# Performance work log

Hardware: AMD Instinct MI355X
Metric: run time of the kernel (lower is better)

The kernel has to match this reference:

```python
import jax, jax.numpy as jnp
import numpy as np

DIM = 1024
HEADS = 16
DIM_HEAD = 64
SCALE = DIM_HEAD ** -0.5
LN_EPS = 1e-5


def rotate_half(x):
    # '... (j d) -> ... j d' with j=2, then cat(-x2, x1)
    d = x.shape[-1] // 2
    x1, x2 = x[..., :d], x[..., d:]
    return jnp.concatenate((-x2, x1), axis=-1)


def apply_rotary_pos_emb(pos, t):
    seq_len, rotate_dim = t.shape[-2], pos.shape[-1]
    pos = pos[..., -seq_len:, :]
    t_rot, t_pass = t[..., :rotate_dim], t[..., rotate_dim:]
    t_rot = t_rot * jnp.cos(pos) + rotate_half(t_rot) * jnp.sin(pos)
    return jnp.concatenate((t_rot, t_pass), axis=-1)


def setup_inputs() -> dict:
    key = jax.random.key(0)
    ks = jax.random.split(key, 4)
    b, n = 2, 2048
    inner = HEADS * DIM_HEAD
    x = jax.random.normal(ks[0], (b, n, DIM), dtype=jnp.float32)
    rotary_pos_emb = jax.random.normal(ks[1], (n, DIM_HEAD), dtype=jnp.float32)
    # params (torch Linear stored transposed here as [in, out])
    w_qkv = jax.random.normal(ks[2], (DIM, inner * 3), dtype=jnp.float32) * (DIM ** -0.5)
    w_out = jax.random.normal(ks[3], (inner, DIM), dtype=jnp.float32) * (inner ** -0.5)
    ln_w = jnp.ones((DIM,), dtype=jnp.float32)
    ln_b = jnp.zeros((DIM,), dtype=jnp.float32)
    return {"x": x, "rotary_pos_emb": rotary_pos_emb, "ln_w": ln_w, "ln_b": ln_b,
            "w_qkv": w_qkv, "w_out": w_out}


def reference(x, rotary_pos_emb, ln_w, ln_b, w_qkv, w_out):
    b, n, _ = x.shape
    # LayerNorm
    mu = jnp.mean(x, axis=-1, keepdims=True)
    var = jnp.mean(jnp.square(x - mu), axis=-1, keepdims=True)
    xn = (x - mu) * jax.lax.rsqrt(var + LN_EPS) * ln_w + ln_b
    # QKV projection
    qkv = xn @ w_qkv  # [b, n, 3*inner]
    q, k, v = jnp.split(qkv, 3, axis=-1)
    split_heads = lambda t: t.reshape(b, n, HEADS, DIM_HEAD).transpose(0, 2, 1, 3)
    q, k, v = split_heads(q), split_heads(k), split_heads(v)  # [b, h, n, d]
    q = q * SCALE
    q = apply_rotary_pos_emb(rotary_pos_emb, q)
    k = apply_rotary_pos_emb(rotary_pos_emb, k)
    sim = jnp.einsum('bhid,bhjd->bhij', q, k)
    causal_mask = jnp.triu(jnp.ones((n, n), dtype=bool), k=1)
    sim = jnp.where(causal_mask, -jnp.finfo(sim.dtype).max, sim)
    attn = jax.nn.softmax(sim, axis=-1)
    out = jnp.einsum('bhij,bhjd->bhid', attn, v)
    out = out.transpose(0, 2, 1, 3).reshape(b, n, HEADS * DIM_HEAD)
    return out @ w_out
```

## Files before the change

kernel.cpp:

```cpp
#include <hip/hip_runtime.h>
#include <hip/hip_bf16.h>

typedef __bf16 bf16;
typedef __attribute__((ext_vector_type(8))) __bf16 bf16x8;
typedef __attribute__((ext_vector_type(4))) __bf16 bf16x4;
typedef __attribute__((ext_vector_type(4))) float f32x4;
typedef __attribute__((ext_vector_type(16))) float f32x16;
typedef __attribute__((ext_vector_type(2))) int int2v;
typedef __attribute__((ext_vector_type(4))) int int4v;

#define HEADS 16
#define DHEAD 64
#define SEQ 2048
#define DIMM 1024
#define QKVN (3*DIMM)
#define SCALEQ 0.125f

__device__ __forceinline__ void gload_lds16(const bf16* g, bf16* l) {
  __builtin_amdgcn_global_load_lds(
      (const __attribute__((address_space(1))) void*)g,
      (__attribute__((address_space(3))) void*)l, 16, 0, 0);
}

__device__ __forceinline__ f32x16 mfma32(bf16x8 a, bf16x8 b, f32x16 c) {
  return __builtin_amdgcn_mfma_f32_32x32x16_bf16(a, b, c, 0, 0, 0);
}

__device__ __forceinline__ unsigned cvtpk(float a, float b) {
  unsigned r;
  asm("v_cvt_pk_bf16_f32 %0, %1, %2" : "=v"(r) : "v"(a), "v"(b));
  return r;
}

__global__ __launch_bounds__(256) void transpose_cast_k(const float* __restrict__ in,
                                                        bf16* __restrict__ out, int R, int C) {
  __shared__ bf16 tile[32][33];
  int bc = blockIdx.x, br = blockIdx.y;
  int t = threadIdx.x;
  int c = t & 31, r0 = t >> 5;
  for (int i = 0; i < 4; i++) {
    int r = r0 + i * 8;
    tile[r][c] = (bf16)in[(size_t)(br * 32 + r) * C + bc * 32 + c];
  }
  __syncthreads();
  for (int i = 0; i < 4; i++) {
    int r = r0 + i * 8;
    out[(size_t)(bc * 32 + r) * R + br * 32 + c] = tile[c][r];
  }
}

__global__ void rope_table_k(const float* __restrict__ pos, float2* __restrict__ cs) {
  int i = blockIdx.x * 256 + threadIdx.x;
  float p = pos[i];
  cs[i] = make_float2(cosf(p), sinf(p));
}

__global__ __launch_bounds__(256) void ln_k(const float* __restrict__ x, const float* __restrict__ w,
                                            const float* __restrict__ bsh, bf16* __restrict__ xn) {
  int row = blockIdx.x, t = threadIdx.x;
  const float4 v = reinterpret_cast<const float4*>(x + (size_t)row * DIMM)[t];
  float s1 = v.x + v.y + v.z + v.w;
  float s2 = v.x * v.x + v.y * v.y + v.z * v.z + v.w * v.w;
  for (int off = 1; off < 64; off <<= 1) {
    s1 += __shfl_xor(s1, off, 64);
    s2 += __shfl_xor(s2, off, 64);
  }
  __shared__ float red[8];
  int wv = t >> 6;
  if ((t & 63) == 0) { red[wv * 2] = s1; red[wv * 2 + 1] = s2; }
  __syncthreads();
  s1 = red[0] + red[2] + red[4] + red[6];
  s2 = red[1] + red[3] + red[5] + red[7];
  float mu = s1 * (1.0f / DIMM);
  float var = s2 * (1.0f / DIMM) - mu * mu;
  float rs = rsqrtf(var + 1e-5f);
  const float4 wv4 = reinterpret_cast<const float4*>(w)[t];
  const float4 bv4 = reinterpret_cast<const float4*>(bsh)[t];
  bf16x4 o;
  o[0] = (bf16)((v.x - mu) * rs * wv4.x + bv4.x);
  o[1] = (bf16)((v.y - mu) * rs * wv4.y + bv4.y);
  o[2] = (bf16)((v.z - mu) * rs * wv4.z + bv4.z);
  o[3] = (bf16)((v.w - mu) * rs * wv4.w + bv4.w);
  *reinterpret_cast<bf16x4*>(xn + (size_t)row * DIMM + t * 4) = o;
}

template<int WRITE_BF16>
__global__ __launch_bounds__(256) void gemm_bt_k(const bf16* __restrict__ A, const bf16* __restrict__ Bt,
                                                 void* __restrict__ Cp, int Ndim, int K) {
  __shared__ bf16 As[128][64];
  __shared__ bf16 Bs[128][64];
  int bn = blockIdx.x, bm = blockIdx.y;
  int t = threadIdx.x, lane = t & 63, wid = t >> 6;
  int lr = lane & 15, lg = lane >> 4;
  int wm = (wid >> 1) * 64, wn = (wid & 1) * 64;
  f32x4 acc[4][4] = {};
  const bf16* Ab = A + (size_t)bm * 128 * K;
  const bf16* Bb = Bt + (size_t)bn * 128 * K;
  for (int k0 = 0; k0 < K; k0 += 64) {
    __syncthreads();
#pragma unroll
    for (int i = 0; i < 4; i++) {
      int ch = i * 256 + t;
      int row = ch >> 3, c8 = (ch & 7) * 8;
      gload_lds16(Ab + (size_t)row * K + k0 + c8, &As[0][0] + ch * 8);
      gload_lds16(Bb + (size_t)row * K + k0 + c8, &Bs[0][0] + ch * 8);
    }
    __syncthreads();
#pragma unroll
    for (int ks = 0; ks < 2; ks++) {
      bf16x8 af[4], bfr[4];
#pragma unroll
      for (int i = 0; i < 4; i++) af[i]  = *reinterpret_cast<const bf16x8*>(&As[wm + i * 16 + lr][ks * 32 + lg * 8]);
#pragma unroll
      for (int i = 0; i < 4; i++) bfr[i] = *reinterpret_cast<const bf16x8*>(&Bs[wn + i * 16 + lr][ks * 32 + lg * 8]);
#pragma unroll
      for (int mi = 0; mi < 4; mi++)
#pragma unroll
        for (int ni = 0; ni < 4; ni++)
          acc[mi][ni] = __builtin_amdgcn_mfma_f32_16x16x32_bf16(af[mi], bfr[ni], acc[mi][ni], 0, 0, 0);
    }
  }
#pragma unroll
  for (int mi = 0; mi < 4; mi++)
#pragma unroll
    for (int ni = 0; ni < 4; ni++)
#pragma unroll
      for (int j = 0; j < 4; j++) {
        size_t r = (size_t)bm * 128 + wm + mi * 16 + lg * 4 + j;
        size_t c = (size_t)bn * 128 + wn + ni * 16 + lr;
        if (WRITE_BF16) reinterpret_cast<bf16*>(Cp)[r * Ndim + c] = (bf16)acc[mi][ni][j];
        else            reinterpret_cast<float*>(Cp)[r * Ndim + c] = acc[mi][ni][j];
      }
}

__global__ __launch_bounds__(256) void frag_all_k(const bf16* __restrict__ qkv, const float2* __restrict__ cs,
                                                  bf16* __restrict__ qf, bf16* __restrict__ kf,
                                                  bf16* __restrict__ vf) {
  __shared__ bf16 tl[3][64][72];
  int jt = blockIdx.x, bh = blockIdx.y;
  int b = bh >> 4, h = bh & 15;
  int t = threadIdx.x;
#pragma unroll
  for (int rep = 0; rep < 6; rep++) {
    int u = rep * 256 + t;
    int sel = u >> 9, w = u & 511;
    int kv = w >> 3, dc = w & 7;
    bf16x8 v = *reinterpret_cast<const bf16x8*>(
        qkv + ((size_t)(b * SEQ + jt * 64 + kv)) * QKVN + sel * DIMM + h * 64 + dc * 8);
    *reinterpret_cast<bf16x8*>(&tl[sel][kv][dc * 8]) = v;
  }
  __syncthreads();
  int lane2 = t & 63;
  int lo = lane2 & 31, hi = lane2 >> 5;
#pragma unroll
  for (int rep = 0; rep < 2; rep++) {
    int sub = rep * 4 + (t >> 6);
    int g4 = sub >> 2, ks = sub & 3;
    int n_l = g4 * 32 + lo;
    int db = ks * 16 + hi * 8;
    int n = jt * 64 + n_l;
    float sg = (db < 32) ? -1.f : 1.f;
    {
      bf16x8 xv = *reinterpret_cast<const bf16x8*>(&tl[0][n_l][db]);
      bf16x8 yv = *reinterpret_cast<const bf16x8*>(&tl[0][n_l][db ^ 32]);
      bf16x8 ov;
#pragma unroll
      for (int e = 0; e < 8; e++) {
        float2 cz = cs[n * 64 + db + e];
        ov[e] = (bf16)(((float)xv[e] * cz.x + sg * (float)yv[e] * cz.y) * SCALEQ);
      }
      *reinterpret_cast<bf16x8*>(qf + ((size_t)((bh * 64 + jt * 2 + g4) * 4 + ks)) * 512 + lane2 * 8) = ov;
    }
    {
      bf16x8 xv = *reinterpret_cast<const bf16x8*>(&tl[1][n_l][db]);
      bf16x8 yv = *reinterpret_cast<const bf16x8*>(&tl[1][n_l][db ^ 32]);
      bf16x8 ov;
#pragma unroll
      for (int e = 0; e < 8; e++) {
        float2 cz = cs[n * 64 + db + e];
        ov[e] = (bf16)((float)xv[e] * cz.x + sg * (float)yv[e] * cz.y);
      }
      *reinterpret_cast<bf16x8*>(kf + ((size_t)((bh * 32 + jt) * 8 + g4 * 4 + ks)) * 512 + lane2 * 8) = ov;
    }
    {
      int d = g4 * 32 + lo, kvb = ks * 16 + hi * 8;
      bf16x8 ov;
#pragma unroll
      for (int e = 0; e < 8; e++) ov[e] = tl[2][kvb + e][d];
      *reinterpret_cast<bf16x8*>(vf + ((size_t)((bh * 32 + jt) * 8 + g4 * 4 + ks)) * 512 + lane2 * 8) = ov;
    }
  }
}

__global__ __launch_bounds__(256, 4) void attn_k(const bf16* __restrict__ qf_g, const bf16* __restrict__ kf_g,
                                                 const bf16* __restrict__ vf_g, bf16* __restrict__ o) {
  __shared__ float ldsO[4][2048];
  __shared__ float ldsM[4][32];
  __shared__ float ldsL[4][32];
  int band = 63 - blockIdx.x;
  int bh = blockIdx.y;
  int b = bh >> 4, h = bh & 15;
  int T = (band >> 1) + 1;
  int t = threadIdx.x, lane = t & 63, w = t >> 6;
  int lo = lane & 31, hi = lane >> 5;
  int qrow0 = band * 32;
  int qg = qrow0 + lo;
  const bf16* qp = qf_g + ((size_t)(bh * 64 + band) * 4) * 512 + lane * 8;
  bf16x8 qfr[4];
#pragma unroll
  for (int ks = 0; ks < 4; ks++) qfr[ks] = *reinterpret_cast<const bf16x8*>(qp + ks * 512);
  f32x16 accO0 = {}, accO1 = {};
  float m_run = -1e30f, l_run = 0.f;
  const bf16* kb = kf_g + (size_t)bh * 32 * 8 * 512 + lane * 8;
  const bf16* vb = vf_g + (size_t)bh * 32 * 8 * 512 + lane * 8;
  for (int jt = w; jt < T; jt += 4) {
    const bf16* kt = kb + (size_t)jt * 8 * 512;
    const bf16* vt = vb + (size_t)jt * 8 * 512;
    bf16x8 ka[8];
#pragma unroll
    for (int u = 0; u < 8; u++) ka[u] = *reinterpret_cast<const bf16x8*>(kt + u * 512);
    f32x16 s0 = {}, s1 = {};
#pragma unroll
    for (int ks = 0; ks < 4; ks++) s0 = mfma32(ka[ks], qfr[ks], s0);
#pragma unroll
    for (int ks = 0; ks < 4; ks++) s1 = mfma32(ka[4 + ks], qfr[ks], s1);
    if (jt == T - 1) {
      int kv0 = jt * 64 + 4 * hi;
#pragma unroll
      for (int r = 0; r < 16; r++) {
        int kvg = kv0 + (r & 3) + 8 * (r >> 2);
        if (kvg > qg) s0[r] = -1e30f;
        if (kvg + 32 > qg) s1[r] = -1e30f;
      }
    }
    float pmax = s0[0];
#pragma unroll
    for (int r = 1; r < 16; r++) pmax = fmaxf(pmax, s0[r]);
#pragma unroll
    for (int r = 0; r < 16; r++) pmax = fmaxf(pmax, s1[r]);
    pmax = fmaxf(pmax, __shfl_xor(pmax, 32, 64));
    if (__any(pmax > m_run + 8.f)) {
      float mn = fmaxf(m_run, pmax);
      float corr = __expf(m_run - mn);
      m_run = mn;
      l_run *= corr;
      if (hi == 0) ldsM[w][lo] = corr;
#pragma unroll
      for (int r = 0; r < 16; r++) {
        float c = ldsM[w][(r & 3) + 8 * (r >> 2) + 4 * hi];
        accO0[r] *= c;
        accO1[r] *= c;
      }
    }
    float rs = 0.f;
#pragma unroll
    for (int r = 0; r < 16; r++) { s0[r] = __expf(s0[r] - m_run); rs += s0[r]; }
#pragma unroll
    for (int r = 0; r < 16; r++) { s1[r] = __expf(s1[r] - m_run); rs += s1[r]; }
    rs += __shfl_xor(rs, 32, 64);
    l_run += rs;
#pragma unroll
    for (int ks = 0; ks < 4; ks++) {
      unsigned a0, a1, b0, b1;
      if (ks == 0) { a0 = cvtpk(s0[0], s0[1]);  a1 = cvtpk(s0[2], s0[3]);
                     b0 = cvtpk(s0[4], s0[5]);  b1 = cvtpk(s0[6], s0[7]); }
      else if (ks == 1) { a0 = cvtpk(s0[8], s0[9]);   a1 = cvtpk(s0[10], s0[11]);
                          b0 = cvtpk(s0[12], s0[13]); b1 = cvtpk(s0[14], s0[15]); }
      else if (ks == 2) { a0 = cvtpk(s1[0], s1[1]);  a1 = cvtpk(s1[2], s1[3]);
                          b0 = cvtpk(s1[4], s1[5]);  b1 = cvtpk(s1[6], s1[7]); }
      else { a0 = cvtpk(s1[8], s1[9]);   a1 = cvtpk(s1[10], s1[11]);
             b0 = cvtpk(s1[12], s1[13]); b1 = cvtpk(s1[14], s1[15]); }
      int2v r0 = __builtin_amdgcn_permlane32_swap((int)a0, (int)b0, false, false);
      int2v r1 = __builtin_amdgcn_permlane32_swap((int)a1, (int)b1, false, false);
      int4v wv; wv[0] = r0[0]; wv[1] = r1[0]; wv[2] = r0[1]; wv[3] = r1[1];
      bf16x8 pa = __builtin_bit_cast(bf16x8, wv);
      bf16x8 v0 = *reinterpret_cast<const bf16x8*>(vt + (0 + ks) * 512);
      bf16x8 v1 = *reinterpret_cast<const bf16x8*>(vt + (4 + ks) * 512);
      accO0 = mfma32(pa, v0, accO0);
      accO1 = mfma32(pa, v1, accO1);
    }
  }
  if (hi == 0) { ldsM[w][lo] = m_run; ldsL[w][lo] = l_run; }
#pragma unroll
  for (int r = 0; r < 16; r++) {
    int q = (r & 3) + 8 * (r >> 2) + 4 * hi;
    ldsO[w][q * 64 + lo] = accO0[r];
    ldsO[w][q * 64 + 32 + lo] = accO1[r];
  }
  __syncthreads();
  {
    int q = t >> 3, d0 = (t & 7) * 8;
    float m0 = ldsM[0][q], m1 = ldsM[1][q], m2 = ldsM[2][q], m3 = ldsM[3][q];
    float mstar = fmaxf(fmaxf(m0, m1), fmaxf(m2, m3));
    float lsum = 0.f;
    float4 oa = make_float4(0.f, 0.f, 0.f, 0.f), ob = oa;
#pragma unroll
    for (int w2 = 0; w2 < 4; w2++) {
      float sc = __expf(ldsM[w2][q] - mstar);
      lsum += sc * ldsL[w2][q];
      const float4* p = reinterpret_cast<const float4*>(&ldsO[w2][q * 64 + d0]);
      float4 pa = p[0], pb = p[1];
      oa.x += sc * pa.x; oa.y += sc * pa.y; oa.z += sc * pa.z; oa.w += sc * pa.w;
      ob.x += sc * pb.x; ob.y += sc * pb.y; ob.z += sc * pb.z; ob.w += sc * pb.w;
    }
    float inv = 1.0f / lsum;
    bf16x8 ov;
    ov[0] = (bf16)(oa.x * inv); ov[1] = (bf16)(oa.y * inv);
    ov[2] = (bf16)(oa.z * inv); ov[3] = (bf16)(oa.w * inv);
    ov[4] = (bf16)(ob.x * inv); ov[5] = (bf16)(ob.y * inv);
    ov[6] = (bf16)(ob.z * inv); ov[7] = (bf16)(ob.w * inv);
    *reinterpret_cast<bf16x8*>(o + ((size_t)(b * SEQ + qrow0 + q)) * DIMM + h * 64 + d0) = ov;
  }
}

extern "C" void kernel_launch(void* const* d_in, const int* in_sizes, int n_in,
                              void* d_out, int out_size, void* d_ws, size_t ws_size,
                              hipStream_t stream) {
  const float* x    = (const float*)d_in[0];
  const float* rpe  = (const float*)d_in[1];
  const float* lnw  = (const float*)d_in[2];
  const float* lnb  = (const float*)d_in[3];
  const float* wqkv = (const float*)d_in[4];
  const float* wout = (const float*)d_in[5];

  char* ws = (char*)d_ws;
  bf16*   xn    = (bf16*)(ws);
  bf16*   wqkvT = (bf16*)(ws + 8388608);
  bf16*   woutT = (bf16*)(ws + 14680064);
  bf16*   qkv   = (bf16*)(ws + 16777216);
  bf16*   qfrag = (bf16*)(ws + 41943040);
  bf16*   kfrag = (bf16*)(ws + 50331648);
  bf16*   vfrag = (bf16*)(ws + 58720256);
  bf16*   obuf  = (bf16*)(ws + 67108864);
  float2* cs    = (float2*)(ws + 75497472);

  transpose_cast_k<<<dim3(96, 32), 256, 0, stream>>>(wqkv, wqkvT, 1024, 3072);
  transpose_cast_k<<<dim3(32, 32), 256, 0, stream>>>(wout, woutT, 1024, 1024);
  rope_table_k<<<512, 256, 0, stream>>>(rpe, cs);
  ln_k<<<4096, 256, 0, stream>>>(x, lnw, lnb, xn);
  gemm_bt_k<1><<<dim3(24, 32), 256, 0, stream>>>(xn, wqkvT, (void*)qkv, 3072, 1024);
  frag_all_k<<<dim3(32, 32), 256, 0, stream>>>(qkv, cs, qfrag, kfrag, vfrag);
  attn_k<<<dim3(64, 32), 256, 0, stream>>>(qfrag, kfrag, vfrag, obuf);
  gemm_bt_k<0><<<dim3(8, 32), 256, 0, stream>>>(obuf, woutT, (float*)d_out, 1024, 1024);
}
```

Before: 236.1 us.

## Add 256x256 pipelined QKV GEMM and halve attention LDS for occupancy

Replaces the 128x128 QKV projection GEMM with a 256x256-tile, 512-thread kernel. It uses a 4-slot global_load_lds pipeline with swizzled LDS, split MFMA phases, and setprio scheduling to raise operand reuse and overlap loads with math. Separately, the attention kernel stores its per-wave partial outputs in bf16 instead of fp32 and raises launch bounds to 8 blocks per CU, trading some precision in the cross-wave merge for more occupancy. The new GEMM launches only 192 blocks, which may underfill the CUs, and its bf16 stores are scalar and poorly coalesced.

```diff
diff --git a/kernel.cpp b/kernel.cpp
--- a/kernel.cpp
+++ b/kernel.cpp
@@ -84,6 +84,97 @@
   *reinterpret_cast<bf16x4*>(xn + (size_t)row * DIMM + t * 4) = o;
 }
 
+__global__ __launch_bounds__(512, 2) void gemm256_k(const bf16* __restrict__ A, const bf16* __restrict__ Bt,
+                                                    bf16* __restrict__ C, int Ndim, int K) {
+  __shared__ bf16 lds[4][2][8192];
+  const int t = threadIdx.x, lane = t & 63, w = t >> 6;
+  const int wr = w >> 2, wc = w & 3;
+  const int lr = lane & 15, lg = lane >> 4;
+  const int bn = blockIdx.x, bm = blockIdx.y;
+  const bf16* Ab = A + (size_t)(bm * 256) * K;
+  const bf16* Bb = Bt + (size_t)(bn * 256) * K;
+  const int nt = K >> 5;
+
+  auto STAGE = [&](int T, int i0, int i1) {
+    int k0 = T << 5;
+    for (int i = i0; i < i1; ++i) {
+      int c = t + i * 512;
+      int Lt = c * 16;
+      int isB = Lt >> 14;
+      int Lh = Lt & 16383;
+      int Ls = Lh ^ (((Lh >> 9) & 1) << 5);
+      int elem = Ls >> 1;
+      int row = elem >> 5, col = elem & 31;
+      const bf16* src = (isB ? Bb : Ab) + (size_t)row * K + k0 + col;
+      gload_lds16(src, &lds[T & 3][isB][0] + (Lh >> 1));
+    }
+  };
+  auto LDA = [&](int slot, int mi) -> bf16x8 {
+    int row = wr * 128 + mi * 16 + lr;
+    int L0 = row * 64 + lg * 16;
+    int L = L0 ^ (((L0 >> 9) & 1) << 5);
+    return *reinterpret_cast<const bf16x8*>(reinterpret_cast<const char*>(&lds[slot][0][0]) + L);
+  };
+  auto LDB = [&](int slot, int ni) -> bf16x8 {
+    int row = wc * 64 + ni * 16 + lr;
+    int L0 = row * 64 + lg * 16;
+    int L = L0 ^ (((L0 >> 9) & 1) << 5);
+    return *reinterpret_cast<const bf16x8*>(reinterpret_cast<const char*>(&lds[slot][1][0]) + L);
+  };
+
+  f32x4 acc[8][4] = {};
+  STAGE(0, 0, 4); STAGE(1, 0, 4); STAGE(2, 0, 4);
+  asm volatile("s_waitcnt vmcnt(8)" ::: "memory");
+  __builtin_amdgcn_s_barrier();
+  __builtin_amdgcn_sched_barrier(0);
+
+  for (int T = 0; T < nt; ++T) {
+    int slot = T & 3;
+    bf16x8 bfr[4], af[4];
+#pragma unroll
+    for (int ni = 0; ni < 4; ni++) bfr[ni] = LDB(slot, ni);
+#pragma unroll
+    for (int mi = 0; mi < 4; mi++) af[mi] = LDA(slot, mi);
+    if (T + 3 < nt) STAGE(T + 3, 0, 2);
+    __builtin_amdgcn_s_setprio(1);
+#pragma unroll
+    for (int mi = 0; mi < 4; mi++)
+#pragma unroll
+      for (int ni = 0; ni < 4; ni++)
+        acc[mi][ni] = __builtin_amdgcn_mfma_f32_16x16x32_bf16(af[mi], bfr[ni], acc[mi][ni], 0, 0, 0);
+    __builtin_amdgcn_s_setprio(0);
+    __builtin_amdgcn_s_barrier();
+#pragma unroll
+    for (int mi = 0; mi < 4; mi++) af[mi] = LDA(slot, 4 + mi);
+    if (T + 3 < nt) STAGE(T + 3, 2, 4);
+    __builtin_amdgcn_s_setprio(1);
+#pragma unroll
+    for (int mi = 0; mi < 4; mi++)
+#pragma unroll
+      for (int ni = 0; ni < 4; ni++)
+        acc[4 + mi][ni] = __builtin_amdgcn_mfma_f32_16x16x32_bf16(af[mi], bfr[ni], acc[4 + mi][ni], 0, 0, 0);
+    __builtin_amdgcn_s_setprio(0);
+    int rem = nt - 1 - T;
+    if (rem > 0) {
+      if (rem >= 3)      asm volatile("s_waitcnt vmcnt(8)" ::: "memory");
+      else if (rem == 2) asm volatile("s_waitcnt vmcnt(4)" ::: "memory");
+      else               asm volatile("s_waitcnt vmcnt(0)" ::: "memory");
+      __builtin_amdgcn_s_barrier();
+      __builtin_amdgcn_sched_barrier(0);
+    }
+  }
+#pragma unroll
+  for (int mi = 0; mi < 8; mi++)
+#pragma unroll
+    for (int ni = 0; ni < 4; ni++)
+#pragma unroll
+      for (int j = 0; j < 4; j++) {
+        size_t r = (size_t)bm * 256 + wr * 128 + mi * 16 + lg * 4 + j;
+        size_t c = (size_t)bn * 256 + wc * 64 + ni * 16 + lr;
+        C[r * Ndim + c] = (bf16)acc[mi][ni][j];
+      }
+}
+
 template<int WRITE_BF16>
 __global__ __launch_bounds__(256) void gemm_bt_k(const bf16* __restrict__ A, const bf16* __restrict__ Bt,
                                                  void* __restrict__ Cp, int Ndim, int K) {
@@ -192,9 +283,9 @@
   }
 }
 
-__global__ __launch_bounds__(256, 4) void attn_k(const bf16* __restrict__ qf_g, const bf16* __restrict__ kf_g,
+__global__ __launch_bounds__(256, 8) void attn_k(const bf16* __restrict__ qf_g, const bf16* __restrict__ kf_g,
                                                  const bf16* __restrict__ vf_g, bf16* __restrict__ o) {
-  __shared__ float ldsO[4][2048];
+  __shared__ bf16 ldsO[4][2048];
   __shared__ float ldsM[4][32];
   __shared__ float ldsL[4][32];
   int band = 63 - blockIdx.x;
@@ -284,8 +375,8 @@
 #pragma unroll
   for (int r = 0; r < 16; r++) {
     int q = (r & 3) + 8 * (r >> 2) + 4 * hi;
-    ldsO[w][q * 64 + lo] = accO0[r];
-    ldsO[w][q * 64 + 32 + lo] = accO1[r];
+    ldsO[w][q * 64 + lo] = (bf16)accO0[r];
+    ldsO[w][q * 64 + 32 + lo] = (bf16)accO1[r];
   }
   __syncthreads();
   {
@@ -293,22 +384,19 @@
     float m0 = ldsM[0][q], m1 = ldsM[1][q], m2 = ldsM[2][q], m3 = ldsM[3][q];
     float mstar = fmaxf(fmaxf(m0, m1), fmaxf(m2, m3));
     float lsum = 0.f;
-    float4 oa = make_float4(0.f, 0.f, 0.f, 0.f), ob = oa;
+    float oacc[8] = {};
 #pragma unroll
     for (int w2 = 0; w2 < 4; w2++) {
       float sc = __expf(ldsM[w2][q] - mstar);
       lsum += sc * ldsL[w2][q];
-      const float4* p = reinterpret_cast<const float4*>(&ldsO[w2][q * 64 + d0]);
-      float4 pa = p[0], pb = p[1];
-      oa.x += sc * pa.x; oa.y += sc * pa.y; oa.z += sc * pa.z; oa.w += sc * pa.w;
-      ob.x += sc * pb.x; ob.y += sc * pb.y; ob.z += sc * pb.z; ob.w += sc * pb.w;
+      bf16x8 pv = *reinterpret_cast<const bf16x8*>(&ldsO[w2][q * 64 + d0]);
+#pragma unroll
+      for (int e = 0; e < 8; e++) oacc[e] += sc * (float)pv[e];
     }
     float inv = 1.0f / lsum;
     bf16x8 ov;
-    ov[0] = (bf16)(oa.x * inv); ov[1] = (bf16)(oa.y * inv);
-    ov[2] = (bf16)(oa.z * inv); ov[3] = (bf16)(oa.w * inv);
-    ov[4] = (bf16)(ob.x * inv); ov[5] = (bf16)(ob.y * inv);
-    ov[6] = (bf16)(ob.z * inv); ov[7] = (bf16)(ob.w * inv);
+#pragma unroll
+    for (int e = 0; e < 8; e++) ov[e] = (bf16)(oacc[e] * inv);
     *reinterpret_cast<bf16x8*>(o + ((size_t)(b * SEQ + qrow0 + q)) * DIMM + h * 64 + d0) = ov;
   }
 }
@@ -338,7 +426,7 @@
   transpose_cast_k<<<dim3(32, 32), 256, 0, stream>>>(wout, woutT, 1024, 1024);
   rope_table_k<<<512, 256, 0, stream>>>(rpe, cs);
   ln_k<<<4096, 256, 0, stream>>>(x, lnw, lnb, xn);
-  gemm_bt_k<1><<<dim3(24, 32), 256, 0, stream>>>(xn, wqkvT, (void*)qkv, 3072, 1024);
+  gemm256_k<<<dim3(12, 16), 512, 0, stream>>>(xn, wqkvT, qkv, 3072, 1024);
   frag_all_k<<<dim3(32, 32), 256, 0, stream>>>(qkv, cs, qfrag, kfrag, vfrag);
   attn_k<<<dim3(64, 32), 256, 0, stream>>>(qfrag, kfrag, vfrag, obuf);
   gemm_bt_k<0><<<dim3(8, 32), 256, 0, stream>>>(obuf, woutT, (float*)d_out, 1024, 1024);
```

Measured after the change: 538.7 us. 2.28x slower.
